# Performance work log

Hardware: AMD Instinct MI355X
Metric: run time of the kernel (lower is better)

The kernel has to match this reference:

```python
import jax, jax.numpy as jnp
import numpy as np

S = 1024          # tokens (prefill)
DIM = 2560
HEAD_DIM = 128
N_HEADS = 20
N_KV = 5
HPG = N_HEADS // N_KV      # heads per kv group = 4
GS = 128                   # weight-scale group size
THETA = 500000.0
EPS = 1e-05
QKV_OUT = (N_HEADS + 2 * N_KV) * HEAD_DIM  # 3840


def setup_inputs() -> dict:
    key = jax.random.key(0)
    ks = jax.random.split(key, 7)
    x = jax.random.normal(ks[0], (S, DIM), jnp.float32)
    # unpacked int2 (ternary) weights, stored as float for the reference math
    w_qkv = jax.random.randint(ks[1], (QKV_OUT, DIM), -1, 2).astype(jnp.float32)
    ws_qkv = jax.random.uniform(ks[2], (QKV_OUT, DIM // GS), jnp.float32, 0.01, 0.05)
    w_o = jax.random.randint(ks[3], (DIM, N_HEADS * HEAD_DIM), -1, 2).astype(jnp.float32)
    ws_o = jax.random.uniform(ks[4], (DIM, N_HEADS * HEAD_DIM // GS), jnp.float32, 0.01, 0.05)
    q_norm_w = 1.0 + 0.02 * jax.random.normal(ks[5], (HEAD_DIM,), jnp.float32)
    k_norm_w = 1.0 + 0.02 * jax.random.normal(ks[6], (HEAD_DIM,), jnp.float32)
    return {"x": x, "w_qkv": w_qkv, "ws_qkv": ws_qkv, "w_o": w_o, "ws_o": ws_o,
            "q_norm_w": q_norm_w, "k_norm_w": k_norm_w}


def _quant_act(x):
    # per-token symmetric int8 quant: s = 127 / max|x| (clamped)
    s = 127.0 / jnp.clip(jnp.max(jnp.abs(x), axis=-1, keepdims=True), 1e-05, None)
    q = jnp.clip(jnp.round(x * s), -128.0, 127.0)
    return q, s


def _bitlinear(x, w, ws):
    # int8 activation x int2 weight GEMM with per-(out,group) dequant scales
    q, s = _quant_act(x)
    w_dq = w * jnp.repeat(ws, GS, axis=1)        # [out, in]
    return (q @ w_dq.T) / s


def _rmsnorm(x, w):
    return x * jax.lax.rsqrt(jnp.mean(x * x, axis=-1, keepdims=True) + EPS) * w


def _rope(x, cos, sin):
    # x: [S, ..., d]; cos/sin: [S, d//2], interleaved-pair (llama) convention
    d2 = x.shape[-1] // 2
    shape = (x.shape[0],) + (1,) * (x.ndim - 2) + (d2,)
    c = cos.reshape(shape)
    s = sin.reshape(shape)
    xr = x.reshape(x.shape[:-1] + (d2, 2))
    x0, x1 = xr[..., 0], xr[..., 1]
    out = jnp.stack([x0 * c - x1 * s, x0 * s + x1 * c], axis=-1)
    return out.reshape(x.shape)


def reference(x, w_qkv, ws_qkv, w_o, ws_o, q_norm_w, k_norm_w):
    qkv = _bitlinear(x, w_qkv, ws_qkv)                       # [S, 3840]
    q_size = N_HEADS * HEAD_DIM
    k_size = N_KV * HEAD_DIM
    xq = qkv[:, :q_size].reshape(S, N_KV, HPG, HEAD_DIM)     # [S, g, h, d]
    xk = qkv[:, q_size:q_size + k_size].reshape(S, N_KV, HEAD_DIM)
    xv = qkv[:, q_size + k_size:].reshape(S, N_KV, HEAD_DIM)
    xq = _rmsnorm(xq, q_norm_w)
    xk = _rmsnorm(xk, k_norm_w)
    # RoPE (prefill: positions 0..S-1)
    pos = jnp.arange(S, dtype=jnp.float32)
    inv_freq = THETA ** (-jnp.arange(0, HEAD_DIM, 2, dtype=jnp.float32) / HEAD_DIM)
    ang = pos[:, None] * inv_freq[None, :]                   # [S, d/2]
    cos, sin = jnp.cos(ang), jnp.sin(ang)
    xq = _rope(xq, cos, sin)
    xk = _rope(xk, cos, sin)
    # GQA causal flash-attention math
    scale = HEAD_DIM ** -0.5
    scores = jnp.einsum('sghd,tgd->ghst', xq, xk) * scale    # [g, h, S, S]
    causal = jnp.tril(jnp.ones((S, S), bool))
    scores = jnp.where(causal, scores, -1e30)
    attn = jax.nn.softmax(scores, axis=-1)
    out = jnp.einsum('ghst,tgd->sghd', attn, xv).reshape(S, N_HEADS * HEAD_DIM)
    return _bitlinear(out, w_o, ws_o)                        # [S, DIM]
```

## Files before the change

kernel.cpp:

```cpp
#include <hip/hip_runtime.h>
#include <hip/hip_bf16.h>
#include <cstdint>
#include <math.h>

#define SEQ 1024
#define DIM 2560
#define HD 128
#define NH 20
#define NKV 5
#define QKV_OUT 3840
#define GS 128

typedef __bf16 bf16;
typedef __bf16 bf16x4 __attribute__((ext_vector_type(4)));
typedef __bf16 bf16x8 __attribute__((ext_vector_type(8)));
typedef float f32x4 __attribute__((ext_vector_type(4)));

template <typename T>
__global__ __launch_bounds__(256) void quant_kernel(
    const T* __restrict__ x, bf16* __restrict__ act,
    float* __restrict__ rs, int cols) {
  const int row = blockIdx.x;
  const int tid = threadIdx.x;
  const T* xr = x + (size_t)row * cols;
  float m = 0.f;
  for (int i = tid; i < cols; i += 256) m = fmaxf(m, fabsf((float)xr[i]));
  for (int off = 32; off; off >>= 1) m = fmaxf(m, __shfl_xor(m, off));
  __shared__ float red[4];
  __shared__ float s_bc;
  if ((tid & 63) == 0) red[tid >> 6] = m;
  __syncthreads();
  if (tid == 0) {
    float mm = fmaxf(fmaxf(red[0], red[1]), fmaxf(red[2], red[3]));
    mm = fmaxf(mm, 1e-5f);
    s_bc = 127.f / mm;
    rs[row] = mm / 127.f;
  }
  __syncthreads();
  const float s = s_bc;
  bf16* ar = act + (size_t)row * cols;
  for (int i = tid; i < cols; i += 256) {
    float q = rintf((float)xr[i] * s);
    q = fminf(fmaxf(q, -128.f), 127.f);
    ar[i] = (bf16)q;
  }
}

__global__ __launch_bounds__(256) void dequant2_kernel(
    const float* __restrict__ w1, const float* __restrict__ ws1, bf16* __restrict__ o1,
    const float* __restrict__ w2, const float* __restrict__ ws2, bf16* __restrict__ o2,
    long n1_4, long total4) {
  long i = (long)blockIdx.x * 256 + threadIdx.x;
  if (i >= total4) return;
  const float* w; const float* ws; bf16* o; long e;
  if (i < n1_4) { w = w1; ws = ws1; o = o1; e = i * 4; }
  else          { w = w2; ws = ws2; o = o2; e = (i - n1_4) * 4; }
  int row = (int)(e / DIM);
  int k = (int)(e % DIM);
  float sc = ws[(size_t)row * (DIM / GS) + (k / GS)];
  float4 wv = *(const float4*)(w + e);
  bf16x4 ov;
  ov[0] = (bf16)(wv.x * sc);
  ov[1] = (bf16)(wv.y * sc);
  ov[2] = (bf16)(wv.z * sc);
  ov[3] = (bf16)(wv.w * sc);
  *(bf16x4*)(o + e) = ov;
}

__device__ __forceinline__ void gload_lds16(const bf16* g, bf16* l) {
  __builtin_amdgcn_global_load_lds(
      (const __attribute__((address_space(1))) void*)g,
      (__attribute__((address_space(3))) void*)l, 16, 0, 0);
}

template <int BM, int BN>
__global__ __launch_bounds__(256) void gemm_pipe(
    const bf16* __restrict__ A, const bf16* __restrict__ B,
    const float* __restrict__ rs, float* __restrict__ C,
    int N, int K, int Kh, size_t part_stride, int ND, int NN) {
  constexpr int MI = BM / 32;
  constexpr int NW = BN / 32;
  constexpr int APASS = BM / 32;
  constexpr int BPASS = BN / 32;
  __shared__ bf16 As[2][BM * 64];
  __shared__ bf16 Bs[2][BN * 64];
  const int b = (int)blockIdx.x;
  const int mtile = b / ND;
  const int nz = b % ND;
  const int ntile = nz % NN;
  const int z = nz / NN;
  const int tid = threadIdx.x;
  const int w = tid >> 6, l = tid & 63;
  const int row0 = mtile * BM;
  const int col0 = ntile * BN;
  const int wm = (w >> 1) * (BM / 2), wn = (w & 1) * (BN / 2);
  const int lcol = l & 15, quad = l >> 4;
  const int sr = l >> 3, sg = l & 7;
  const bf16* Ag = A + (size_t)row0 * K + (size_t)z * Kh;
  const bf16* Bg = B + (size_t)col0 * K + (size_t)z * Kh;

  f32x4 acc[MI][NW] = {};

#define STAGE_AB(buf, k0)                                                      \
  {                                                                            \
    _Pragma("unroll") for (int i = 0; i < APASS; ++i) {                        \
      int rb = w * (BM / 4) + i * 8;                                           \
      int r = rb + sr;                                                         \
      gload_lds16(Ag + (size_t)r * K + (k0) + ((sg ^ (r & 7)) * 8),            \
                  &As[buf][rb * 64]);                                          \
    }                                                                          \
    _Pragma("unroll") for (int i = 0; i < BPASS; ++i) {                        \
      int rb = w * (BN / 4) + i * 8;                                           \
      int r = rb + sr;                                                         \
      gload_lds16(Bg + (size_t)r * K + (k0) + ((sg ^ (r & 7)) * 8),            \
                  &Bs[buf][rb * 64]);                                          \
    }                                                                          \
  }

  STAGE_AB(0, 0)
  __syncthreads();

  int buf = 0;
  for (int k0 = 0; k0 < Kh; k0 += 64) {
    if (k0 + 64 < Kh) STAGE_AB(buf ^ 1, k0 + 64)
#pragma unroll
    for (int ks = 0; ks < 2; ++ks) {
      bf16x8 af[MI], bff[NW];
#pragma unroll
      for (int mi = 0; mi < MI; ++mi) {
        int R = wm + mi * 16 + lcol;
        af[mi] = *(const bf16x8*)(&As[buf][R * 64 + (((ks * 4 + quad) ^ (R & 7)) * 8)]);
      }
#pragma unroll
      for (int ni = 0; ni < NW; ++ni) {
        int R = wn + ni * 16 + lcol;
        bff[ni] = *(const bf16x8*)(&Bs[buf][R * 64 + (((ks * 4 + quad) ^ (R & 7)) * 8)]);
      }
#pragma unroll
      for (int mi = 0; mi < MI; ++mi)
#pragma unroll
        for (int ni = 0; ni < NW; ++ni)
          acc[mi][ni] = __builtin_amdgcn_mfma_f32_16x16x32_bf16(
              af[mi], bff[ni], acc[mi][ni], 0, 0, 0);
    }
    __syncthreads();
    buf ^= 1;
  }
#undef STAGE_AB

  float* Cp = C + (size_t)z * part_stride;
#pragma unroll
  for (int mi = 0; mi < MI; ++mi) {
#pragma unroll
    for (int ni = 0; ni < NW; ++ni) {
      int col = col0 + wn + ni * 16 + lcol;
#pragma unroll
      for (int r = 0; r < 4; ++r) {
        int row = row0 + wm + mi * 16 + quad * 4 + r;
        Cp[(size_t)row * N + col] = acc[mi][ni][r] * rs[row];
      }
    }
  }
}

__global__ void qk_post(const float* __restrict__ qkvA, const float* __restrict__ qkvB,
                        const float* __restrict__ qw, const float* __restrict__ kw,
                        bf16* __restrict__ Qo, bf16* __restrict__ Ko) {
  const int t = blockIdx.x, h = blockIdx.y, i = threadIdx.x;
  const size_t off = (h < NH)
      ? (size_t)t * QKV_OUT + h * HD
      : (size_t)t * QKV_OUT + 2560 + (h - NH) * HD;
  const float* s1 = qkvA + off;
  const float* s2 = qkvB + off;
  float x0 = s1[2 * i] + s2[2 * i];
  float x1 = s1[2 * i + 1] + s2[2 * i + 1];
  float ss = x0 * x0 + x1 * x1;
  for (int off2 = 1; off2 < 64; off2 <<= 1) ss += __shfl_xor(ss, off2);
  float r = rsqrtf(ss * (1.f / 128.f) + 1e-5f);
  const float* wv = (h < NH) ? qw : kw;
  float y0 = x0 * r * wv[2 * i];
  float y1 = x1 * r * wv[2 * i + 1];
  float inv_freq = powf(500000.f, -(float)(2 * i) * (1.f / 128.f));
  float ang = (float)t * inv_freq;
  float sn, cs;
  sincosf(ang, &sn, &cs);
  float o0 = y0 * cs - y1 * sn;
  float o1 = y0 * sn + y1 * cs;
  if (h < NH) {
    bf16* dst = Qo + ((size_t)t * NH + h) * HD + 2 * i;
    dst[0] = (bf16)o0; dst[1] = (bf16)o1;
  } else {
    bf16* dst = Ko + ((size_t)(h - NH) * SEQ + t) * HD + 2 * i;
    dst[0] = (bf16)o0; dst[1] = (bf16)o1;
  }
}

__global__ __launch_bounds__(256) void v_post(const float* __restrict__ qkvA,
                                              const float* __restrict__ qkvB,
                                              bf16* __restrict__ Vt) {
  const int t0 = blockIdx.x * 64, g = blockIdx.y;
  const int tid = threadIdx.x;
  __shared__ bf16 Ls[64 * 137];
  {
    const int tl = tid >> 4;
    const int d0 = (tid & 15) * 8;
#pragma unroll
    for (int pass = 0; pass < 4; ++pass) {
      int t = pass * 16 + tl;
      size_t off = (size_t)(t0 + t) * QKV_OUT + 3200 + g * HD + d0;
      float4 a = *(const float4*)(qkvA + off);
      float4 b = *(const float4*)(qkvA + off + 4);
      float4 a2 = *(const float4*)(qkvB + off);
      float4 b2 = *(const float4*)(qkvB + off + 4);
      bf16* dst = Ls + t * 137 + d0;
      dst[0] = (bf16)(a.x + a2.x); dst[1] = (bf16)(a.y + a2.y);
      dst[2] = (bf16)(a.z + a2.z); dst[3] = (bf16)(a.w + a2.w);
      dst[4] = (bf16)(b.x + b2.x); dst[5] = (bf16)(b.y + b2.y);
      dst[6] = (bf16)(b.z + b2.z); dst[7] = (bf16)(b.w + b2.w);
    }
  }
  __syncthreads();
  {
    const int dl = tid >> 3;
    const int tl0 = (tid & 7) * 8;
#pragma unroll
    for (int pass = 0; pass < 4; ++pass) {
      int d = pass * 32 + dl;
      bf16x8 v;
#pragma unroll
      for (int j = 0; j < 8; ++j) v[j] = Ls[(tl0 + j) * 137 + d];
      *(bf16x8*)(Vt + ((size_t)g * HD + d) * SEQ + t0 + tl0) = v;
    }
  }
}

__global__ __launch_bounds__(256) void attn_mfma(
    const bf16* __restrict__ Qb, const bf16* __restrict__ Kb,
    const bf16* __restrict__ Vt, bf16* __restrict__ O) {
  const int qb = 31 - (int)blockIdx.x;
  const int hp = blockIdx.y;
  const int tid = threadIdx.x;
  const int wave = tid >> 6, lane = tid & 63;
  const int H = (hp >> 1) * 4 + (hp & 1) * 2 + (wave >> 1);
  const int g = H >> 2;
  const int qcol = lane & 15, quad = lane >> 4;
  const int q_tok = qb * 32 + (wave & 1) * 16 + qcol;
  const float scale = 0.08838834764831843f;

  __shared__ bf16 Ks[2][64 * 128];
  __shared__ bf16 Vs[2][128 * 64];

  const bf16* kbase = Kb + (size_t)g * SEQ * HD;
  const bf16* vbase = Vt + (size_t)g * HD * SEQ;

  bf16x8 qf[4];
  {
    const bf16* qp = Qb + ((size_t)q_tok * NH + H) * HD + quad * 8;
#pragma unroll
    for (int kc = 0; kc < 4; ++kc) qf[kc] = *(const bf16x8*)(qp + kc * 32);
  }

  float m_i = -1e30f, l_i = 0.f;
  f32x4 o_acc[8] = {};
  const int kt_max = (qb * 32 + 31) >> 6;

  const int k_r = lane >> 4, k_g = lane & 15;
  const int v_r = lane >> 3, v_g = lane & 7;

#define STAGE(buf, key0)                                                       \
  {                                                                            \
    _Pragma("unroll") for (int p = 0; p < 4; ++p) {                            \
      int r0 = wave * 16 + p * 4;                                              \
      int r = r0 + k_r;                                                        \
      gload_lds16(kbase + (size_t)((key0) + r) * HD + ((k_g ^ (r & 15)) * 8),  \
                  &Ks[buf][r0 * 128]);                                         \
    }                                                                          \
    _Pragma("unroll") for (int p = 0; p < 4; ++p) {                            \
      int r0 = wave * 32 + p * 8;                                              \
      int r = r0 + v_r;                                                        \
      gload_lds16(vbase + (size_t)r * SEQ + (key0) + ((v_g ^ (r & 7)) * 8),    \
                  &Vs[buf][r0 * 64]);                                          \
    }                                                                          \
  }

  STAGE(0, 0)

  for (int kt = 0; kt <= kt_max; ++kt) {
    const int key0 = kt * 64;
    __syncthreads();
    if (kt < kt_max) STAGE((kt + 1) & 1, key0 + 64)
    const bf16* Kt = Ks[kt & 1];
    const bf16* Vtile = Vs[kt & 1];

    f32x4 s[4];
#pragma unroll
    for (int mg = 0; mg < 4; ++mg) {
      const int R = mg * 16 + qcol;
      const bf16* krow = Kt + R * 128;
      f32x4 acc = {0.f, 0.f, 0.f, 0.f};
#pragma unroll
      for (int kc = 0; kc < 4; ++kc) {
        int j = kc * 4 + quad;
        bf16x8 kf = *(const bf16x8*)(krow + ((j ^ (R & 15)) * 8));
        acc = __builtin_amdgcn_mfma_f32_16x16x32_bf16(kf, qf[kc], acc, 0, 0, 0);
      }
      s[mg] = acc;
    }

    float mt = -1e30f;
#pragma unroll
    for (int mg = 0; mg < 4; ++mg)
#pragma unroll
      for (int r = 0; r < 4; ++r) {
        int key = key0 + mg * 16 + quad * 4 + r;
        float v = (key <= q_tok) ? s[mg][r] * scale : -1e30f;
        s[mg][r] = v;
        mt = fmaxf(mt, v);
      }
    mt = fmaxf(mt, __shfl_xor(mt, 16));
    mt = fmaxf(mt, __shfl_xor(mt, 32));
    float mnew = fmaxf(m_i, mt);
    float alpha = __expf(m_i - mnew);
    float ps = 0.f;
#pragma unroll
    for (int mg = 0; mg < 4; ++mg)
#pragma unroll
      for (int r = 0; r < 4; ++r) {
        float pv = __expf(s[mg][r] - mnew);
        s[mg][r] = pv;
        ps += pv;
      }
    ps += __shfl_xor(ps, 16);
    ps += __shfl_xor(ps, 32);
    l_i = l_i * alpha + ps;
    m_i = mnew;
#pragma unroll
    for (int mg2 = 0; mg2 < 8; ++mg2)
#pragma unroll
      for (int r = 0; r < 4; ++r) o_acc[mg2][r] *= alpha;

    bf16x8 pb[2];
#pragma unroll
    for (int c = 0; c < 2; ++c)
#pragma unroll
      for (int j = 0; j < 8; ++j)
        pb[c][j] = (bf16)s[c * 2 + (j >> 2)][j & 3];

#pragma unroll
    for (int mg2 = 0; mg2 < 8; ++mg2) {
      const int R = mg2 * 16 + qcol;
      const bf16* vrow = Vtile + R * 64;
      f32x4 acc = o_acc[mg2];
#pragma unroll
      for (int c = 0; c < 2; ++c) {
        int g8a = c * 8 + quad;
        int g8b = c * 8 + 4 + quad;
        bf16x4 v0 = *(const bf16x4*)(vrow + ((g8a >> 1) ^ (R & 7)) * 8 + (g8a & 1) * 4);
        bf16x4 v1 = *(const bf16x4*)(vrow + ((g8b >> 1) ^ (R & 7)) * 8 + (g8b & 1) * 4);
        bf16x8 vfr;
#pragma unroll
        for (int j = 0; j < 4; ++j) { vfr[j] = v0[j]; vfr[j + 4] = v1[j]; }
        acc = __builtin_amdgcn_mfma_f32_16x16x32_bf16(vfr, pb[c], acc, 0, 0, 0);
      }
      o_acc[mg2] = acc;
    }
  }
#undef STAGE

  const float inv = 1.f / l_i;
  bf16* op = O + (size_t)q_tok * DIM + H * HD + quad * 4;
#pragma unroll
  for (int mg2 = 0; mg2 < 8; ++mg2) {
    bf16x4 vv;
    vv[0] = (bf16)(o_acc[mg2][0] * inv);
    vv[1] = (bf16)(o_acc[mg2][1] * inv);
    vv[2] = (bf16)(o_acc[mg2][2] * inv);
    vv[3] = (bf16)(o_acc[mg2][3] * inv);
    *(bf16x4*)(op + mg2 * 16) = vv;
  }
}

extern "C" void kernel_launch(void* const* d_in, const int* in_sizes, int n_in,
                              void* d_out, int out_size, void* d_ws, size_t ws_size,
                              hipStream_t stream) {
  const float* x      = (const float*)d_in[0];
  const float* w_qkv  = (const float*)d_in[1];
  const float* ws_qkv = (const float*)d_in[2];
  const float* w_o    = (const float*)d_in[3];
  const float* ws_o   = (const float*)d_in[4];
  const float* qnw    = (const float*)d_in[5];
  const float* knw    = (const float*)d_in[6];
  float* out = (float*)d_out;

  char* p = (char*)d_ws;
  bf16*  act1 = (bf16*)p;  p += (size_t)SEQ * DIM * 2;
  float* rs1  = (float*)p; p += 4096;
  bf16*  wqdq = (bf16*)p;  p += (size_t)QKV_OUT * DIM * 2;
  bf16*  wodq = (bf16*)p;  p += (size_t)DIM * DIM * 2;
  float* qkvA = (float*)p; p += (size_t)SEQ * QKV_OUT * 4;
  float* qkvB = (float*)p; p += (size_t)SEQ * QKV_OUT * 4;
  bf16*  Qb   = (bf16*)p;  p += (size_t)SEQ * NH * HD * 2;
  bf16*  Kb   = (bf16*)p;  p += (size_t)NKV * SEQ * HD * 2;
  bf16*  Vt   = (bf16*)p;  p += (size_t)NKV * HD * SEQ * 2;
  bf16*  attn = (bf16*)p;  p += (size_t)SEQ * DIM * 2;
  bf16*  act2 = (bf16*)p;  p += (size_t)SEQ * DIM * 2;
  float* rs2  = (float*)p; p += 4096;

  quant_kernel<float><<<SEQ, 256, 0, stream>>>(x, act1, rs1, DIM);
  {
    long n1_4 = (long)QKV_OUT * DIM / 4;
    long total4 = n1_4 + (long)DIM * DIM / 4;
    dequant2_kernel<<<(int)((total4 + 255) / 256), 256, 0, stream>>>(
        w_qkv, ws_qkv, wqdq, w_o, ws_o, wodq, n1_4, total4);
  }
  gemm_pipe<128, 128><<<480, 256, 0, stream>>>(
      act1, wqdq, rs1, qkvA, QKV_OUT, DIM, DIM / 2, (size_t)SEQ * QKV_OUT, 60, 30);
  qk_post<<<dim3(SEQ, 25), 64, 0, stream>>>(qkvA, qkvB, qnw, knw, Qb, Kb);
  v_post<<<dim3(SEQ / 64, NKV), 256, 0, stream>>>(qkvA, qkvB, Vt);
  attn_mfma<<<dim3(32, 10), 256, 0, stream>>>(Qb, Kb, Vt, attn);
  quant_kernel<bf16><<<SEQ, 256, 0, stream>>>(attn, act2, rs2, DIM);
  gemm_pipe<64, 64><<<640, 256, 0, stream>>>(
      act2, wodq, rs2, out, DIM, DIM, DIM, 0, 40, 40);
}
```

Before: 239.2 us.

## Fuse pre/post elementwise kernels and hoist K/V LDS loads in attention

Merges the activation quantization and weight dequantization into one launch, and merges the Q/K norm+RoPE and V transpose kernels into one launch, with the qk part now packing 4 rows per 256-thread block. Cutting two launches and the gaps between them is meant to reduce fixed per-kernel overhead. In attention, all K and V fragments for a tile are loaded from LDS up front, ahead of the MFMA and softmax work, so load latency can overlap with compute. The kernel is also marked launch_bounds(256,1). Holding all fragments raises register pressure, which the occupancy hint allows at the cost of fewer waves.

```diff
diff --git a/kernel.cpp b/kernel.cpp
--- a/kernel.cpp
+++ b/kernel.cpp
@@ -46,25 +46,53 @@
   }
 }
 
-__global__ __launch_bounds__(256) void dequant2_kernel(
+__global__ __launch_bounds__(256) void fused_pre(
+    const float* __restrict__ x, bf16* __restrict__ act, float* __restrict__ rs,
     const float* __restrict__ w1, const float* __restrict__ ws1, bf16* __restrict__ o1,
     const float* __restrict__ w2, const float* __restrict__ ws2, bf16* __restrict__ o2,
     long n1_4, long total4) {
-  long i = (long)blockIdx.x * 256 + threadIdx.x;
-  if (i >= total4) return;
-  const float* w; const float* ws; bf16* o; long e;
-  if (i < n1_4) { w = w1; ws = ws1; o = o1; e = i * 4; }
-  else          { w = w2; ws = ws2; o = o2; e = (i - n1_4) * 4; }
-  int row = (int)(e / DIM);
-  int k = (int)(e % DIM);
-  float sc = ws[(size_t)row * (DIM / GS) + (k / GS)];
-  float4 wv = *(const float4*)(w + e);
-  bf16x4 ov;
-  ov[0] = (bf16)(wv.x * sc);
-  ov[1] = (bf16)(wv.y * sc);
-  ov[2] = (bf16)(wv.z * sc);
-  ov[3] = (bf16)(wv.w * sc);
-  *(bf16x4*)(o + e) = ov;
+  const int tid = threadIdx.x;
+  if (blockIdx.x < SEQ) {
+    const int row = blockIdx.x;
+    const float* xr = x + (size_t)row * DIM;
+    float m = 0.f;
+    for (int i = tid; i < DIM; i += 256) m = fmaxf(m, fabsf(xr[i]));
+    for (int off = 32; off; off >>= 1) m = fmaxf(m, __shfl_xor(m, off));
+    __shared__ float red[4];
+    __shared__ float s_bc;
+    if ((tid & 63) == 0) red[tid >> 6] = m;
+    __syncthreads();
+    if (tid == 0) {
+      float mm = fmaxf(fmaxf(red[0], red[1]), fmaxf(red[2], red[3]));
+      mm = fmaxf(mm, 1e-5f);
+      s_bc = 127.f / mm;
+      rs[row] = mm / 127.f;
+    }
+    __syncthreads();
+    const float s = s_bc;
+    bf16* ar = act + (size_t)row * DIM;
+    for (int i = tid; i < DIM; i += 256) {
+      float q = rintf(xr[i] * s);
+      q = fminf(fmaxf(q, -128.f), 127.f);
+      ar[i] = (bf16)q;
+    }
+  } else {
+    long i = (long)(blockIdx.x - SEQ) * 256 + tid;
+    if (i >= total4) return;
+    const float* w; const float* ws; bf16* o; long e;
+    if (i < n1_4) { w = w1; ws = ws1; o = o1; e = i * 4; }
+    else          { w = w2; ws = ws2; o = o2; e = (i - n1_4) * 4; }
+    int row = (int)(e / DIM);
+    int k = (int)(e % DIM);
+    float sc = ws[(size_t)row * (DIM / GS) + (k / GS)];
+    float4 wv = *(const float4*)(w + e);
+    bf16x4 ov;
+    ov[0] = (bf16)(wv.x * sc);
+    ov[1] = (bf16)(wv.y * sc);
+    ov[2] = (bf16)(wv.z * sc);
+    ov[3] = (bf16)(wv.w * sc);
+    *(bf16x4*)(o + e) = ov;
+  }
 }
 
 __device__ __forceinline__ void gload_lds16(const bf16* g, bf16* l) {
@@ -163,78 +191,81 @@
   }
 }
 
-__global__ void qk_post(const float* __restrict__ qkvA, const float* __restrict__ qkvB,
-                        const float* __restrict__ qw, const float* __restrict__ kw,
-                        bf16* __restrict__ Qo, bf16* __restrict__ Ko) {
-  const int t = blockIdx.x, h = blockIdx.y, i = threadIdx.x;
-  const size_t off = (h < NH)
-      ? (size_t)t * QKV_OUT + h * HD
-      : (size_t)t * QKV_OUT + 2560 + (h - NH) * HD;
-  const float* s1 = qkvA + off;
-  const float* s2 = qkvB + off;
-  float x0 = s1[2 * i] + s2[2 * i];
-  float x1 = s1[2 * i + 1] + s2[2 * i + 1];
-  float ss = x0 * x0 + x1 * x1;
-  for (int off2 = 1; off2 < 64; off2 <<= 1) ss += __shfl_xor(ss, off2);
-  float r = rsqrtf(ss * (1.f / 128.f) + 1e-5f);
-  const float* wv = (h < NH) ? qw : kw;
-  float y0 = x0 * r * wv[2 * i];
-  float y1 = x1 * r * wv[2 * i + 1];
-  float inv_freq = powf(500000.f, -(float)(2 * i) * (1.f / 128.f));
-  float ang = (float)t * inv_freq;
-  float sn, cs;
-  sincosf(ang, &sn, &cs);
-  float o0 = y0 * cs - y1 * sn;
-  float o1 = y0 * sn + y1 * cs;
-  if (h < NH) {
-    bf16* dst = Qo + ((size_t)t * NH + h) * HD + 2 * i;
-    dst[0] = (bf16)o0; dst[1] = (bf16)o1;
+__global__ __launch_bounds__(256) void fused_post(
+    const float* __restrict__ qkvA, const float* __restrict__ qkvB,
+    const float* __restrict__ qw, const float* __restrict__ kw,
+    bf16* __restrict__ Qo, bf16* __restrict__ Ko, bf16* __restrict__ Vt) {
+  __shared__ bf16 Ls[64 * 137];
+  const int bx = (int)blockIdx.x;
+  const int tid = threadIdx.x;
+  if (bx < 6400) {
+    const int wave = tid >> 6, i = tid & 63;
+    const int u = bx * 4 + wave;
+    const int t = u & 1023, h = u >> 10;
+    const size_t off = (h < NH)
+        ? (size_t)t * QKV_OUT + h * HD
+        : (size_t)t * QKV_OUT + 2560 + (h - NH) * HD;
+    const float* s1 = qkvA + off;
+    const float* s2 = qkvB + off;
+    float x0 = s1[2 * i] + s2[2 * i];
+    float x1 = s1[2 * i + 1] + s2[2 * i + 1];
+    float ss = x0 * x0 + x1 * x1;
+    for (int off2 = 1; off2 < 64; off2 <<= 1) ss += __shfl_xor(ss, off2);
+    float r = rsqrtf(ss * (1.f / 128.f) + 1e-5f);
+    const float* wv = (h < NH) ? qw : kw;
+    float y0 = x0 * r * wv[2 * i];
+    float y1 = x1 * r * wv[2 * i + 1];
+    float inv_freq = powf(500000.f, -(float)(2 * i) * (1.f / 128.f));
+    float ang = (float)t * inv_freq;
+    float sn, cs;
+    sincosf(ang, &sn, &cs);
+    float o0 = y0 * cs - y1 * sn;
+    float o1 = y0 * sn + y1 * cs;
+    if (h < NH) {
+      bf16* dst = Qo + ((size_t)t * NH + h) * HD + 2 * i;
+      dst[0] = (bf16)o0; dst[1] = (bf16)o1;
+    } else {
+      bf16* dst = Ko + ((size_t)(h - NH) * SEQ + t) * HD + 2 * i;
+      dst[0] = (bf16)o0; dst[1] = (bf16)o1;
+    }
   } else {
-    bf16* dst = Ko + ((size_t)(h - NH) * SEQ + t) * HD + 2 * i;
-    dst[0] = (bf16)o0; dst[1] = (bf16)o1;
-  }
-}
-
-__global__ __launch_bounds__(256) void v_post(const float* __restrict__ qkvA,
-                                              const float* __restrict__ qkvB,
-                                              bf16* __restrict__ Vt) {
-  const int t0 = blockIdx.x * 64, g = blockIdx.y;
-  const int tid = threadIdx.x;
-  __shared__ bf16 Ls[64 * 137];
-  {
-    const int tl = tid >> 4;
-    const int d0 = (tid & 15) * 8;
-#pragma unroll
-    for (int pass = 0; pass < 4; ++pass) {
-      int t = pass * 16 + tl;
-      size_t off = (size_t)(t0 + t) * QKV_OUT + 3200 + g * HD + d0;
-      float4 a = *(const float4*)(qkvA + off);
-      float4 b = *(const float4*)(qkvA + off + 4);
-      float4 a2 = *(const float4*)(qkvB + off);
-      float4 b2 = *(const float4*)(qkvB + off + 4);
-      bf16* dst = Ls + t * 137 + d0;
-      dst[0] = (bf16)(a.x + a2.x); dst[1] = (bf16)(a.y + a2.y);
-      dst[2] = (bf16)(a.z + a2.z); dst[3] = (bf16)(a.w + a2.w);
-      dst[4] = (bf16)(b.x + b2.x); dst[5] = (bf16)(b.y + b2.y);
-      dst[6] = (bf16)(b.z + b2.z); dst[7] = (bf16)(b.w + b2.w);
-    }
-  }
-  __syncthreads();
-  {
-    const int dl = tid >> 3;
-    const int tl0 = (tid & 7) * 8;
-#pragma unroll
-    for (int pass = 0; pass < 4; ++pass) {
-      int d = pass * 32 + dl;
-      bf16x8 v;
-#pragma unroll
-      for (int j = 0; j < 8; ++j) v[j] = Ls[(tl0 + j) * 137 + d];
-      *(bf16x8*)(Vt + ((size_t)g * HD + d) * SEQ + t0 + tl0) = v;
-    }
-  }
-}
-
-__global__ __launch_bounds__(256) void attn_mfma(
+    const int b2 = bx - 6400;
+    const int t0 = (b2 & 15) * 64, g = b2 >> 4;
+    {
+      const int tl = tid >> 4;
+      const int d0 = (tid & 15) * 8;
+#pragma unroll
+      for (int pass = 0; pass < 4; ++pass) {
+        int t = pass * 16 + tl;
+        size_t off = (size_t)(t0 + t) * QKV_OUT + 3200 + g * HD + d0;
+        float4 a = *(const float4*)(qkvA + off);
+        float4 b = *(const float4*)(qkvA + off + 4);
+        float4 a2 = *(const float4*)(qkvB + off);
+        float4 b2v = *(const float4*)(qkvB + off + 4);
+        bf16* dst = Ls + t * 137 + d0;
+        dst[0] = (bf16)(a.x + a2.x); dst[1] = (bf16)(a.y + a2.y);
+        dst[2] = (bf16)(a.z + a2.z); dst[3] = (bf16)(a.w + a2.w);
+        dst[4] = (bf16)(b.x + b2v.x); dst[5] = (bf16)(b.y + b2v.y);
+        dst[6] = (bf16)(b.z + b2v.z); dst[7] = (bf16)(b.w + b2v.w);
+      }
+    }
+    __syncthreads();
+    {
+      const int dl = tid >> 3;
+      const int tl0 = (tid & 7) * 8;
+#pragma unroll
+      for (int pass = 0; pass < 4; ++pass) {
+        int d = pass * 32 + dl;
+        bf16x8 v;
+#pragma unroll
+        for (int j = 0; j < 8; ++j) v[j] = Ls[(tl0 + j) * 137 + d];
+        *(bf16x8*)(Vt + ((size_t)g * HD + d) * SEQ + t0 + tl0) = v;
+      }
+    }
+  }
+}
+
+__global__ __launch_bounds__(256, 1) void attn_mfma(
     const bf16* __restrict__ Qb, const bf16* __restrict__ Kb,
     const bf16* __restrict__ Vt, bf16* __restrict__ O) {
   const int qb = 31 - (int)blockIdx.x;
@@ -292,19 +323,39 @@
     const bf16* Kt = Ks[kt & 1];
     const bf16* Vtile = Vs[kt & 1];
 
-    f32x4 s[4];
+    bf16x8 kf[4][4];
 #pragma unroll
     for (int mg = 0; mg < 4; ++mg) {
       const int R = mg * 16 + qcol;
       const bf16* krow = Kt + R * 128;
+#pragma unroll
+      for (int kc = 0; kc < 4; ++kc)
+        kf[mg][kc] = *(const bf16x8*)(krow + (((kc * 4 + quad) ^ (R & 15)) * 8));
+    }
+    f32x4 s[4];
+#pragma unroll
+    for (int mg = 0; mg < 4; ++mg) {
       f32x4 acc = {0.f, 0.f, 0.f, 0.f};
 #pragma unroll
-      for (int kc = 0; kc < 4; ++kc) {
-        int j = kc * 4 + quad;
-        bf16x8 kf = *(const bf16x8*)(krow + ((j ^ (R & 15)) * 8));
-        acc = __builtin_amdgcn_mfma_f32_16x16x32_bf16(kf, qf[kc], acc, 0, 0, 0);
-      }
+      for (int kc = 0; kc < 4; ++kc)
+        acc = __builtin_amdgcn_mfma_f32_16x16x32_bf16(kf[mg][kc], qf[kc], acc, 0, 0, 0);
       s[mg] = acc;
+    }
+
+    bf16x8 vf[8][2];
+#pragma unroll
+    for (int mg2 = 0; mg2 < 8; ++mg2) {
+      const int R = mg2 * 16 + qcol;
+      const bf16* vrow = Vtile + R * 64;
+#pragma unroll
+      for (int c = 0; c < 2; ++c) {
+        int g8a = c * 8 + quad;
+        int g8b = c * 8 + 4 + quad;
+        bf16x4 v0 = *(const bf16x4*)(vrow + ((g8a >> 1) ^ (R & 7)) * 8 + (g8a & 1) * 4);
+        bf16x4 v1 = *(const bf16x4*)(vrow + ((g8b >> 1) ^ (R & 7)) * 8 + (g8b & 1) * 4);
+#pragma unroll
+        for (int j = 0; j < 4; ++j) { vf[mg2][c][j] = v0[j]; vf[mg2][c][j + 4] = v1[j]; }
+      }
     }
 
     float mt = -1e30f;
@@ -348,20 +399,10 @@
 
 #pragma unroll
     for (int mg2 = 0; mg2 < 8; ++mg2) {
-      const int R = mg2 * 16 + qcol;
-      const bf16* vrow = Vtile + R * 64;
       f32x4 acc = o_acc[mg2];
 #pragma unroll
-      for (int c = 0; c < 2; ++c) {
-        int g8a = c * 8 + quad;
-        int g8b = c * 8 + 4 + quad;
-        bf16x4 v0 = *(const bf16x4*)(vrow + ((g8a >> 1) ^ (R & 7)) * 8 + (g8a & 1) * 4);
-        bf16x4 v1 = *(const bf16x4*)(vrow + ((g8b >> 1) ^ (R & 7)) * 8 + (g8b & 1) * 4);
-        bf16x8 vfr;
-#pragma unroll
-        for (int j = 0; j < 4; ++j) { vfr[j] = v0[j]; vfr[j + 4] = v1[j]; }
-        acc = __builtin_amdgcn_mfma_f32_16x16x32_bf16(vfr, pb[c], acc, 0, 0, 0);
-      }
+      for (int c = 0; c < 2; ++c)
+        acc = __builtin_amdgcn_mfma_f32_16x16x32_bf16(vf[mg2][c], pb[c], acc, 0, 0, 0);
       o_acc[mg2] = acc;
     }
   }
@@ -406,17 +447,16 @@
   bf16*  act2 = (bf16*)p;  p += (size_t)SEQ * DIM * 2;
   float* rs2  = (float*)p; p += 4096;
 
-  quant_kernel<float><<<SEQ, 256, 0, stream>>>(x, act1, rs1, DIM);
   {
     long n1_4 = (long)QKV_OUT * DIM / 4;
     long total4 = n1_4 + (long)DIM * DIM / 4;
-    dequant2_kernel<<<(int)((total4 + 255) / 256), 256, 0, stream>>>(
-        w_qkv, ws_qkv, wqdq, w_o, ws_o, wodq, n1_4, total4);
+    int dq_blocks = (int)((total4 + 255) / 256);
+    fused_pre<<<SEQ + dq_blocks, 256, 0, stream>>>(
+        x, act1, rs1, w_qkv, ws_qkv, wqdq, w_o, ws_o, wodq, n1_4, total4);
   }
   gemm_pipe<128, 128><<<480, 256, 0, stream>>>(
       act1, wqdq, rs1, qkvA, QKV_OUT, DIM, DIM / 2, (size_t)SEQ * QKV_OUT, 60, 30);
-  qk_post<<<dim3(SEQ, 25), 64, 0, stream>>>(qkvA, qkvB, qnw, knw, Qb, Kb);
-  v_post<<<dim3(SEQ / 64, NKV), 256, 0, stream>>>(qkvA, qkvB, Vt);
+  fused_post<<<6480, 256, 0, stream>>>(qkvA, qkvB, qnw, knw, Qb, Kb, Vt);
   attn_mfma<<<dim3(32, 10), 256, 0, stream>>>(Qb, Kb, Vt, attn);
   quant_kernel<bf16><<<SEQ, 256, 0, stream>>>(attn, act2, rs2, DIM);
   gemm_pipe<64, 64><<<640, 256, 0, stream>>>(
```

New measurement: 232.4 us. 1.03x faster.
